# Kernel tuning notes

Hardware: AMD Instinct MI355X
Metric: run time of the kernel (lower is better)

Reference implementation:

```python
import jax, jax.numpy as jnp
import numpy as np

N = 100000
E = 1600000
IN_C = 128
HID = 32
HEADS = 4
OUT_C = 16
G = 128
NEG_SLOPE = 0.2


def setup_inputs() -> dict:
    key = jax.random.key(0)
    ks = jax.random.split(key, 16)
    x = jax.random.normal(ks[0], (N, IN_C), dtype=jnp.float32)
    edge_index = jax.random.randint(ks[1], (2, E), 0, N, dtype=jnp.int64)
    batch = jnp.sort(jax.random.randint(ks[2], (N,), 0, G, dtype=jnp.int64))
    node_weights = jax.random.uniform(ks[3], (N, 1), dtype=jnp.float32)
    s = 1.0 / np.sqrt(IN_C)
    W1 = jax.random.uniform(ks[4], (IN_C, HEADS * HID), jnp.float32, -s, s)
    att_src1 = jax.random.uniform(ks[5], (HEADS, HID), jnp.float32, -s, s)
    att_dst1 = jax.random.uniform(ks[6], (HEADS, HID), jnp.float32, -s, s)
    b1 = jnp.zeros((HEADS * HID,), jnp.float32)
    s2 = 1.0 / np.sqrt(HEADS * HID)
    W2 = jax.random.uniform(ks[7], (HEADS * HID, HID), jnp.float32, -s2, s2)
    att_src2 = jax.random.uniform(ks[8], (1, HID), jnp.float32, -s2, s2)
    att_dst2 = jax.random.uniform(ks[9], (1, HID), jnp.float32, -s2, s2)
    b2 = jnp.zeros((HID,), jnp.float32)
    s3 = 1.0 / np.sqrt(HID)
    fcW = jax.random.uniform(ks[10], (HID, OUT_C), jnp.float32, -s3, s3)
    fcb = jax.random.uniform(ks[11], (OUT_C,), jnp.float32, -s3, s3)
    return {"x": x, "edge_index": edge_index, "batch": batch,
            "node_weights": node_weights,
            "W1": W1, "att_src1": att_src1, "att_dst1": att_dst1, "b1": b1,
            "W2": W2, "att_src2": att_src2, "att_dst2": att_dst2, "b2": b2,
            "fcW": fcW, "fcb": fcb}


def gat_conv(x, src, dst, W, att_src, att_dst, bias, heads, ch, concat):
    n = x.shape[0]
    h = (x @ W).reshape(n, heads, ch)                       # [N,H,C]
    a_src = jnp.sum(h * att_src[None], axis=-1)             # [N,H]
    a_dst = jnp.sum(h * att_dst[None], axis=-1)             # [N,H]
    e = jax.nn.leaky_relu(a_src[src] + a_dst[dst], NEG_SLOPE)  # [E,H]
    # segment softmax over incoming edges of each destination node
    e_max = jax.ops.segment_max(e, dst, num_segments=n)
    ex = jnp.exp(e - e_max[dst])
    denom = jax.ops.segment_sum(ex, dst, num_segments=n)
    alpha = ex / denom[dst]                                 # [E,H]
    msg = h[src] * alpha[..., None]                         # [E,H,C]
    out = jax.ops.segment_sum(msg, dst, num_segments=n)     # [N,H,C]
    if concat:
        out = out.reshape(n, heads * ch)
    else:
        out = out.mean(axis=1)
    return out + bias


def reference(x, edge_index, batch, node_weights,
              W1, att_src1, att_dst1, b1,
              W2, att_src2, att_dst2, b2,
              fcW, fcb):
    n = x.shape[0]
    # PyG GATConv adds self-loops by default
    loop = jnp.arange(n, dtype=edge_index.dtype)
    src = jnp.concatenate([edge_index[0], loop])
    dst = jnp.concatenate([edge_index[1], loop])

    h = x * node_weights
    h = jax.nn.elu(gat_conv(h, src, dst, W1, att_src1, att_dst1, b1, HEADS, HID, True))
    h = jax.nn.elu(gat_conv(h, src, dst, W2, att_src2, att_dst2, b2, 1, HID, False))
    # global mean pool over graphs
    sums = jax.ops.segment_sum(h, batch, num_segments=G)
    cnts = jax.ops.segment_sum(jnp.ones((n,), h.dtype), batch, num_segments=G)
    pooled = sums / jnp.maximum(cnts, 1.0)[:, None]
    return pooled @ fcW + fcb
```

## Files before the change

### kernel.cpp

```cpp
#include <hip/hip_runtime.h>
#include <cstdint>

#define NGRAPH 128
#define NEG 0.2f
#define NB_MAX 512
#define BSH 8
#define BSZ 256
#define CAP 8192
#define BINCH 2048

typedef unsigned int uint;
typedef unsigned short ushort;
typedef unsigned char uchar;
typedef __attribute__((ext_vector_type(8))) short bf16x8;
typedef __attribute__((ext_vector_type(4))) float f32x4;
typedef __attribute__((ext_vector_type(2))) float f32x2;

union U4B { uint4 u; bf16x8 v; };

__device__ __forceinline__ ushort f2bf(float f) {
  uint u = __float_as_uint(f);
  uint r = (u + 0x7FFF + ((u >> 16) & 1)) >> 16;
  return (ushort)r;
}

__device__ __forceinline__ int wave_incl_scan_i(int v) {
  int lane = threadIdx.x & 63;
#pragma unroll
  for (int off = 1; off < 64; off <<= 1) {
    int u = __shfl_up(v, off, 64);
    if (lane >= off) v += u;
  }
  return v;
}

__global__ void k_bin(const int* __restrict__ ei,
                      const float* __restrict__ W1, const float* __restrict__ W2,
                      ushort* __restrict__ Wt1, ushort* __restrict__ Wt2,
                      int E, int Etot, int NB, int nbin,
                      int* __restrict__ bcur, uint* __restrict__ bbuf) {
  if (blockIdx.x >= (uint)nbin) {
    int t2 = (blockIdx.x - nbin) * 256 + threadIdx.x;
    if (t2 < 16384) {
      int n = t2 >> 7, k = t2 & 127;
      Wt1[t2] = f2bf(W1[k * 128 + n]);
    } else {
      int u = t2 - 16384;
      int n = u >> 7, k = u & 127;
      Wt2[u] = f2bf(W2[k * 32 + n]);
    }
    return;
  }
  __shared__ int h[NB_MAX];
  __shared__ int baseo[NB_MAX];
  int t = threadIdx.x;
  for (int b = t; b < NB; b += 256) h[b] = 0;
  int cbase = blockIdx.x * BINCH;
  int myd[8], mys[8];
#pragma unroll
  for (int j = 0; j < 8; j++) {
    int e = cbase + j * 256 + t;
    if (e < Etot) {
      if (e < E) { mys[j] = ei[e]; myd[j] = ei[E + e]; }
      else { mys[j] = e - E; myd[j] = e - E; }
    } else { myd[j] = -1; mys[j] = 0; }
  }
  __syncthreads();
#pragma unroll
  for (int j = 0; j < 8; j++)
    if (myd[j] >= 0) atomicAdd(&h[myd[j] >> BSH], 1);
  __syncthreads();
  for (int b = t; b < NB; b += 256) {
    int c = h[b];
    baseo[b] = c ? atomicAdd(&bcur[b], c) : 0;
    h[b] = 0;
  }
  __syncthreads();
#pragma unroll
  for (int j = 0; j < 8; j++) {
    if (myd[j] >= 0) {
      int b = myd[j] >> BSH;
      int r = atomicAdd(&h[b], 1);
      bbuf[(size_t)b * CAP + baseo[b] + r] =
          ((uint)(myd[j] & (BSZ - 1)) << 17) | (uint)mys[j];
    }
  }
}

__global__ void k_bg(const uint* __restrict__ bbuf, const int* __restrict__ bcur,
                     int NB, int N, int* __restrict__ offs, int* __restrict__ ssrc,
                     const float* __restrict__ x, const ushort* __restrict__ Wt,
                     const float* __restrict__ nw, const float* __restrict__ att_s,
                     const float* __restrict__ att_d, uchar* __restrict__ hb1,
                     float* __restrict__ asrc, float* __restrict__ adst) {
  __shared__ int sst[NB_MAX + 1];
  __shared__ int wsum2[4];
  __shared__ int deg[BSZ];
  if (blockIdx.x < (uint)NB) {
    int t = threadIdx.x, lane = t & 63, wid = t >> 6;
    int v0 = (2 * t < NB) ? bcur[2 * t] : 0;
    int v1 = (2 * t + 1 < NB) ? bcur[2 * t + 1] : 0;
    int s = v0 + v1;
    int sv = wave_incl_scan_i(s);
    if (lane == 63) wsum2[wid] = sv;
    deg[t] = 0;
    __syncthreads();
    if (t == 0) {
      int r = 0;
#pragma unroll
      for (int k = 0; k < 4; k++) { int x2 = wsum2[k]; wsum2[k] = r; r += x2; }
    }
    __syncthreads();
    int excl = wsum2[wid] + sv - s;
    sst[2 * t] = excl;
    sst[2 * t + 1] = excl + v0;
    if (t == 255) sst[512] = excl + v0 + v1;
    __syncthreads();
    int b = blockIdx.x;
    int ebeg = sst[b], eend = sst[b + 1];
    int cnt = eend - ebeg;
    for (int i = t; i < cnt; i += BSZ)
      atomicAdd(&deg[bbuf[(size_t)b * CAP + i] >> 17], 1);
    __syncthreads();
    int v = deg[t];
    int sv2 = wave_incl_scan_i(v);
    if (lane == 63) wsum2[wid] = sv2;
    __syncthreads();
    if (t == 0) {
      int r = 0;
#pragma unroll
      for (int k = 0; k < 4; k++) { int x2 = wsum2[k]; wsum2[k] = r; r += x2; }
    }
    __syncthreads();
    int excl2 = wsum2[wid] + sv2 - v;
    int node = (b << BSH) + t;
    if (node < N) offs[node] = ebeg + excl2;
    if (b == 0 && t == 0) offs[N] = sst[512];
    __syncthreads();
    deg[t] = excl2;
    __syncthreads();
    for (int i = t; i < cnt; i += BSZ) {
      uint rec = bbuf[(size_t)b * CAP + i];
      int r = atomicAdd(&deg[rec >> 17], 1);
      ssrc[ebeg + r] = (int)(rec & 0x1FFFF);
    }
    return;
  }
  int bid = blockIdx.x - NB;
  int wv = threadIdx.x >> 6, l = threadIdx.x & 63;
  int lg = l >> 4, lr = l & 15;
  int row0 = bid * 64 + wv * 16;
  int node = row0 + lr;
  bool valid = node < N;
  float sc = valid ? nw[node] : 0.f;
  bf16x8 xfr[4];
  const float* xr = x + (size_t)node * 128;
#pragma unroll
  for (int kc = 0; kc < 4; kc++) {
    float v[8];
    if (valid) {
      float4 q0 = *reinterpret_cast<const float4*>(xr + kc * 32 + lg * 8);
      float4 q1 = *reinterpret_cast<const float4*>(xr + kc * 32 + lg * 8 + 4);
      v[0] = q0.x; v[1] = q0.y; v[2] = q0.z; v[3] = q0.w;
      v[4] = q1.x; v[5] = q1.y; v[6] = q1.z; v[7] = q1.w;
    } else {
#pragma unroll
      for (int j = 0; j < 8; j++) v[j] = 0.f;
    }
    U4B a;
    uint pk0 = (uint)f2bf(v[0] * sc) | ((uint)f2bf(v[1] * sc) << 16);
    uint pk1 = (uint)f2bf(v[2] * sc) | ((uint)f2bf(v[3] * sc) << 16);
    uint pk2 = (uint)f2bf(v[4] * sc) | ((uint)f2bf(v[5] * sc) << 16);
    uint pk3 = (uint)f2bf(v[6] * sc) | ((uint)f2bf(v[7] * sc) << 16);
    a.u = make_uint4(pk0, pk1, pk2, pk3);
    xfr[kc] = a.v;
  }
  float pS[4] = {}, pD[4] = {};
#pragma unroll
  for (int ct = 0; ct < 8; ct++) {
    f32x4 acc = {0.f, 0.f, 0.f, 0.f};
    const ushort* wrow = Wt + (size_t)(ct * 16 + lr) * 128;
#pragma unroll
    for (int kc = 0; kc < 4; kc++) {
      U4B bfr;
      bfr.u = *reinterpret_cast<const uint4*>(wrow + kc * 32 + lg * 8);
      acc = __builtin_amdgcn_mfma_f32_16x16x32_bf16(bfr.v, xfr[kc], acc, 0, 0, 0);
    }
    int c0 = ct * 16 + lg * 4;
    if (valid) {
      uint u8 = (uint)__builtin_amdgcn_cvt_pk_fp8_f32(acc[0], acc[1], 0, false);
      u8 = (uint)__builtin_amdgcn_cvt_pk_fp8_f32(acc[2], acc[3], u8, true);
      *reinterpret_cast<uint*>(hb1 + (size_t)node * 128 + c0) = u8;
    }
    float4 as4 = *reinterpret_cast<const float4*>(att_s + c0);
    float4 ad4 = *reinterpret_cast<const float4*>(att_d + c0);
    int h = ct >> 1;
    pS[h] += acc[0] * as4.x + acc[1] * as4.y + acc[2] * as4.z + acc[3] * as4.w;
    pD[h] += acc[0] * ad4.x + acc[1] * ad4.y + acc[2] * ad4.z + acc[3] * ad4.w;
  }
#pragma unroll
  for (int off = 16; off < 64; off <<= 1) {
#pragma unroll
    for (int h = 0; h < 4; h++) {
      pS[h] += __shfl_xor(pS[h], off, 64);
      pD[h] += __shfl_xor(pD[h], off, 64);
    }
  }
  if (lg == 0 && valid) {
    *reinterpret_cast<float4*>(asrc + node * 4) = make_float4(pS[0], pS[1], pS[2], pS[3]);
    *reinterpret_cast<float4*>(adst + node * 4) = make_float4(pD[0], pD[1], pD[2], pD[3]);
  }
}

__global__ void k_aggr1(const int* __restrict__ offs, const int* __restrict__ ssrc,
                        const uchar* __restrict__ hb, const float* __restrict__ asrc,
                        const float* __restrict__ adst, const float* __restrict__ bias,
                        const ushort* __restrict__ Wt2, const float* __restrict__ as2,
                        const float* __restrict__ ad2, uchar* __restrict__ hb2,
                        float* __restrict__ asrc2, float* __restrict__ adst2, int N) {
  __shared__ ushort rowl[4][160];
  int tid = threadIdx.x;
  int wv = tid >> 6, l = tid & 63;
  int d = blockIdx.x * 4 + wv;
  int dc = min(d, N - 1);
  int slot = l >> 3;
  int cb = l & 7;
  int h = cb >> 1;
  float ad = adst[dc * 4 + h];
  int beg = offs[dc], end = offs[dc + 1];
  float a[16] = {};
  float ds = 0.f;
  for (int i = beg; i < end; i += 8) {
    int e = i + slot;
    int ec = min(e, end - 1);
    int s = ssrc[ec];
    float xv = asrc[s * 4 + h] + ad;
    xv = xv > 0.f ? xv : NEG * xv;
    float w = __expf(xv);
    w = (e < end) ? w : 0.f;
    uint4 p = *reinterpret_cast<const uint4*>(hb + (size_t)s * 128 + cb * 16);
    uint pu[4] = {p.x, p.y, p.z, p.w};
#pragma unroll
    for (int q = 0; q < 4; q++) {
      f32x2 f0 = __builtin_amdgcn_cvt_pk_f32_fp8(pu[q], false);
      f32x2 f1 = __builtin_amdgcn_cvt_pk_f32_fp8(pu[q], true);
      a[q * 4 + 0] += w * f0.x;
      a[q * 4 + 1] += w * f0.y;
      a[q * 4 + 2] += w * f1.x;
      a[q * 4 + 3] += w * f1.y;
    }
    ds += w;
  }
  int b3 = (l >> 3) & 1, b4 = (l >> 4) & 1, b5 = (l >> 5) & 1;
  float t8[8];
#pragma unroll
  for (int r = 0; r < 8; r++) {
    float send = b3 ? a[r] : a[r + 8];
    float recv = __shfl_xor(send, 8, 64);
    t8[r] = (b3 ? a[r + 8] : a[r]) + recv;
  }
  float t4[4];
#pragma unroll
  for (int r = 0; r < 4; r++) {
    float send = b4 ? t8[r] : t8[r + 4];
    float recv = __shfl_xor(send, 16, 64);
    t4[r] = (b4 ? t8[r + 4] : t8[r]) + recv;
  }
  float t2[2];
#pragma unroll
  for (int r = 0; r < 2; r++) {
    float send = b5 ? t4[r] : t4[r + 2];
    float recv = __shfl_xor(send, 32, 64);
    t2[r] = (b5 ? t4[r + 2] : t4[r]) + recv;
  }
  ds += __shfl_xor(ds, 8, 64);
  ds += __shfl_xor(ds, 16, 64);
  ds += __shfl_xor(ds, 32, 64);
  float inv = 1.f / (ds > 0.f ? ds : 1.f);
  int c0 = cb * 16 + b3 * 8 + b4 * 4 + b5 * 2;
  float r0 = t2[0] * inv + bias[c0];
  float r1 = t2[1] * inv + bias[c0 + 1];
  r0 = r0 > 0.f ? r0 : expm1f(r0);
  r1 = r1 > 0.f ? r1 : expm1f(r1);
  *reinterpret_cast<uint*>(&rowl[wv][c0]) = (uint)f2bf(r0) | ((uint)f2bf(r1) << 16);
  __syncthreads();
  if (wv != 0) return;
  int lg = l >> 4, lr = l & 15;
  int rsel = lr & 3;
  bf16x8 bfrag[4];
#pragma unroll
  for (int kc = 0; kc < 4; kc++) {
    U4B bb;
    bb.u = *reinterpret_cast<const uint4*>(&rowl[rsel][kc * 32 + lg * 8]);
    bfrag[kc] = bb.v;
  }
  int dd = blockIdx.x * 4 + lr;
  bool vs = (lr < 4) && (dd < N);
  float pS = 0.f, pD = 0.f;
#pragma unroll
  for (int ct = 0; ct < 2; ct++) {
    f32x4 acc = {0.f, 0.f, 0.f, 0.f};
    const ushort* wrow = Wt2 + (size_t)(ct * 16 + lr) * 128;
#pragma unroll
    for (int kc = 0; kc < 4; kc++) {
      U4B bfr;
      bfr.u = *reinterpret_cast<const uint4*>(wrow + kc * 32 + lg * 8);
      acc = __builtin_amdgcn_mfma_f32_16x16x32_bf16(bfr.v, bfrag[kc], acc, 0, 0, 0);
    }
    int cg = ct * 16 + lg * 4;
    if (vs) {
      uint u8 = (uint)__builtin_amdgcn_cvt_pk_fp8_f32(acc[0], acc[1], 0, false);
      u8 = (uint)__builtin_amdgcn_cvt_pk_fp8_f32(acc[2], acc[3], u8, true);
      *reinterpret_cast<uint*>(hb2 + (size_t)dd * 32 + cg) = u8;
    }
    float4 as4 = *reinterpret_cast<const float4*>(as2 + cg);
    float4 ad4 = *reinterpret_cast<const float4*>(ad2 + cg);
    pS += acc[0] * as4.x + acc[1] * as4.y + acc[2] * as4.z + acc[3] * as4.w;
    pD += acc[0] * ad4.x + acc[1] * ad4.y + acc[2] * ad4.z + acc[3] * ad4.w;
  }
  pS += __shfl_xor(pS, 16, 64);
  pS += __shfl_xor(pS, 32, 64);
  pD += __shfl_xor(pD, 16, 64);
  pD += __shfl_xor(pD, 32, 64);
  if (vs && lg == 0) { asrc2[dd] = pS; adst2[dd] = pD; }
}

__global__ void k_aggr2(const int* __restrict__ offs, const int* __restrict__ ssrc,
                        const uchar* __restrict__ hb, const float* __restrict__ asrc,
                        const float* __restrict__ adst, const float* __restrict__ bias,
                        float* __restrict__ out, int N) {
  int wid = threadIdx.x >> 6, l = threadIdx.x & 63;
  int d = blockIdx.x * 4 + wid;
  if (d >= N) return;
  int slot = l >> 2;
  int k = l & 3;
  float ad = adst[d];
  int beg = offs[d], end = offs[d + 1];
  float a[8] = {};
  float ds = 0.f;
  for (int i = beg; i < end; i += 16) {
    int e = i + slot;
    int ec = min(e, end - 1);
    int s = ssrc[ec];
    float xv = asrc[s] + ad;
    xv = xv > 0.f ? xv : NEG * xv;
    float w = __expf(xv);
    w = (e < end) ? w : 0.f;
    uint2 p = *reinterpret_cast<const uint2*>(hb + (size_t)s * 32 + k * 8);
    f32x2 f0 = __builtin_amdgcn_cvt_pk_f32_fp8(p.x, false);
    f32x2 f1 = __builtin_amdgcn_cvt_pk_f32_fp8(p.x, true);
    f32x2 f2 = __builtin_amdgcn_cvt_pk_f32_fp8(p.y, false);
    f32x2 f3 = __builtin_amdgcn_cvt_pk_f32_fp8(p.y, true);
    a[0] += w * f0.x; a[1] += w * f0.y; a[2] += w * f1.x; a[3] += w * f1.y;
    a[4] += w * f2.x; a[5] += w * f2.y; a[6] += w * f3.x; a[7] += w * f3.y;
    ds += w;
  }
  int b2 = (l >> 2) & 1, b3 = (l >> 3) & 1, b4 = (l >> 4) & 1;
  float t4[4];
#pragma unroll
  for (int r = 0; r < 4; r++) {
    float send = b2 ? a[r] : a[r + 4];
    float recv = __shfl_xor(send, 4, 64);
    t4[r] = (b2 ? a[r + 4] : a[r]) + recv;
  }
  float t2[2];
#pragma unroll
  for (int r = 0; r < 2; r++) {
    float send = b3 ? t4[r] : t4[r + 2];
    float recv = __shfl_xor(send, 8, 64);
    t2[r] = (b3 ? t4[r + 2] : t4[r]) + recv;
  }
  float send = b4 ? t2[0] : t2[1];
  float recv = __shfl_xor(send, 16, 64);
  float t1 = (b4 ? t2[1] : t2[0]) + recv;
  t1 += __shfl_xor(t1, 32, 64);
  ds += __shfl_xor(ds, 4, 64);
  ds += __shfl_xor(ds, 8, 64);
  ds += __shfl_xor(ds, 16, 64);
  ds += __shfl_xor(ds, 32, 64);
  if (l < 32) {
    int c = k * 8 + b2 * 4 + b3 * 2 + b4;
    float r = t1 / ds + bias[c];
    r = r > 0.f ? r : expm1f(r);
    out[(size_t)d * 32 + c] = r;
  }
}

__global__ void k_pool_fc(const float* __restrict__ h2, const int* __restrict__ batch,
                          const float* __restrict__ fcW, const float* __restrict__ fcb,
                          float* __restrict__ out, int N) {
  int g = blockIdx.x;
  int lo = 0, hi = N;
  while (lo < hi) { int mid = (lo + hi) >> 1; if (batch[mid] < g) lo = mid + 1; else hi = mid; }
  int beg = lo;
  hi = N;
  while (lo < hi) { int mid = (lo + hi) >> 1; if (batch[mid] < g + 1) lo = mid + 1; else hi = mid; }
  int end = lo;
  int t = threadIdx.x, c = t & 31, sub = t >> 5;
  float acc = 0.f;
  for (int n = beg + sub; n < end; n += 8) acc += h2[(size_t)n * 32 + c];
  __shared__ float red[8][32];
  __shared__ float pooled[32];
  red[sub][c] = acc;
  __syncthreads();
  if (sub == 0) {
    float s = 0.f;
#pragma unroll
    for (int i = 0; i < 8; i++) s += red[i][c];
    float cnt = (float)(end - beg);
    pooled[c] = s / fmaxf(cnt, 1.f);
  }
  __syncthreads();
  if (t < 16) {
    float r = fcb[t];
#pragma unroll
    for (int cc = 0; cc < 32; cc++) r += pooled[cc] * fcW[cc * 16 + t];
    out[g * 16 + t] = r;
  }
}

extern "C" void kernel_launch(void* const* d_in, const int* in_sizes, int n_in,
                              void* d_out, int out_size, void* d_ws, size_t ws_size,
                              hipStream_t stream) {
  const float* x     = (const float*)d_in[0];
  const int*   ei    = (const int*)d_in[1];
  const int*   batch = (const int*)d_in[2];
  const float* nw    = (const float*)d_in[3];
  const float* W1    = (const float*)d_in[4];
  const float* as1w  = (const float*)d_in[5];
  const float* ad1w  = (const float*)d_in[6];
  const float* b1    = (const float*)d_in[7];
  const float* W2    = (const float*)d_in[8];
  const float* as2w  = (const float*)d_in[9];
  const float* ad2w  = (const float*)d_in[10];
  const float* b2    = (const float*)d_in[11];
  const float* fcW   = (const float*)d_in[12];
  const float* fcb   = (const float*)d_in[13];
  float* out = (float*)d_out;

  const int N = in_sizes[0] / 128;
  const int E = in_sizes[1] / 2;
  const int Etot = E + N;
  const int NB = (N + BSZ - 1) >> BSH;

  char* w = (char*)d_ws;
  size_t ofs = 0;
  auto alloc = [&](size_t bytes) {
    char* p = w + ofs;
    ofs += (bytes + 255) & ~(size_t)255;
    return p;
  };
  uchar*  hb1    = (uchar*)alloc((size_t)N * 128);
  uchar*  hb2    = (uchar*)alloc((size_t)N * 32);
  float*  h2     = (float*)alloc((size_t)N * 32 * 4);
  float*  asrc1  = (float*)alloc((size_t)N * 4 * 4);
  float*  adst1  = (float*)alloc((size_t)N * 4 * 4);
  float*  asrc2  = (float*)alloc((size_t)N * 4);
  float*  adst2  = (float*)alloc((size_t)N * 4);
  ushort* Wt1    = (ushort*)alloc(16384 * 2);
  ushort* Wt2    = (ushort*)alloc(4096 * 2);
  int*    bcur   = (int*)alloc((size_t)NB * 4);
  int*    offs   = (int*)alloc((size_t)(N + 1) * 4);
  uint*   bbuf   = (uint*)alloc((size_t)NB * CAP * 4);
  int*    ssrc   = (int*)alloc((size_t)Etot * 4);

  hipMemsetAsync(bcur, 0, (size_t)NB * 4, stream);

  const int nbin = (Etot + BINCH - 1) / BINCH;
  k_bin<<<nbin + 80, 256, 0, stream>>>(ei, W1, W2, Wt1, Wt2, E, Etot, NB, nbin, bcur, bbuf);

  const int ngemm1 = (N + 63) / 64;
  k_bg<<<NB + ngemm1, 256, 0, stream>>>(bbuf, bcur, NB, N, offs, ssrc,
                                        x, Wt1, nw, as1w, ad1w, hb1, asrc1, adst1);

  k_aggr1<<<(N + 3) / 4, 256, 0, stream>>>(offs, ssrc, hb1, asrc1, adst1, b1,
                                           Wt2, as2w, ad2w, hb2, asrc2, adst2, N);

  k_aggr2<<<(N + 3) / 4, 256, 0, stream>>>(offs, ssrc, hb2, asrc2, adst2, b2, h2, N);

  k_pool_fc<<<NGRAPH, 256, 0, stream>>>(h2, batch, fcW, fcb, out, N);
}
```

Before: 314.1 us.

## Fuse global mean pool and FC into aggr2 via atomics and last-block reduction

Instead of writing the full layer-2 activations to memory and running a separate pooling kernel, each node's result is atomically added into a per-graph pooled buffer. A global counter identifies the last block, which computes graph counts and applies the final linear layer. This removes the 12.8 MB intermediate write/read and one launch. In exchange it adds heavy atomic contention, because the sorted batch makes nearby nodes hit the same graph addresses, and it makes the summation order nondeterministic.

```diff
diff --git a/kernel.cpp b/kernel.cpp
--- a/kernel.cpp
+++ b/kernel.cpp
@@ -2,6 +2,7 @@
 #include <cstdint>
 
 #define NGRAPH 128
+#define OUT_C 16
 #define NEG 0.2f
 #define NB_MAX 512
 #define BSH 8
@@ -328,94 +329,100 @@
 __global__ void k_aggr2(const int* __restrict__ offs, const int* __restrict__ ssrc,
                         const uchar* __restrict__ hb, const float* __restrict__ asrc,
                         const float* __restrict__ adst, const float* __restrict__ bias,
-                        float* __restrict__ out, int N) {
+                        const int* __restrict__ batch, const float* __restrict__ fcW,
+                        const float* __restrict__ fcb, float* __restrict__ pooled,
+                        int* __restrict__ counter, float* __restrict__ out,
+                        int N, int nblk) {
+  __shared__ float pl[NGRAPH * 32];
+  __shared__ float cnts[NGRAPH];
+  __shared__ int lastf;
   int wid = threadIdx.x >> 6, l = threadIdx.x & 63;
   int d = blockIdx.x * 4 + wid;
-  if (d >= N) return;
-  int slot = l >> 2;
-  int k = l & 3;
-  float ad = adst[d];
-  int beg = offs[d], end = offs[d + 1];
-  float a[8] = {};
-  float ds = 0.f;
-  for (int i = beg; i < end; i += 16) {
-    int e = i + slot;
-    int ec = min(e, end - 1);
-    int s = ssrc[ec];
-    float xv = asrc[s] + ad;
-    xv = xv > 0.f ? xv : NEG * xv;
-    float w = __expf(xv);
-    w = (e < end) ? w : 0.f;
-    uint2 p = *reinterpret_cast<const uint2*>(hb + (size_t)s * 32 + k * 8);
-    f32x2 f0 = __builtin_amdgcn_cvt_pk_f32_fp8(p.x, false);
-    f32x2 f1 = __builtin_amdgcn_cvt_pk_f32_fp8(p.x, true);
-    f32x2 f2 = __builtin_amdgcn_cvt_pk_f32_fp8(p.y, false);
-    f32x2 f3 = __builtin_amdgcn_cvt_pk_f32_fp8(p.y, true);
-    a[0] += w * f0.x; a[1] += w * f0.y; a[2] += w * f1.x; a[3] += w * f1.y;
-    a[4] += w * f2.x; a[5] += w * f2.y; a[6] += w * f3.x; a[7] += w * f3.y;
-    ds += w;
-  }
-  int b2 = (l >> 2) & 1, b3 = (l >> 3) & 1, b4 = (l >> 4) & 1;
-  float t4[4];
-#pragma unroll
-  for (int r = 0; r < 4; r++) {
-    float send = b2 ? a[r] : a[r + 4];
-    float recv = __shfl_xor(send, 4, 64);
-    t4[r] = (b2 ? a[r + 4] : a[r]) + recv;
-  }
-  float t2[2];
-#pragma unroll
-  for (int r = 0; r < 2; r++) {
-    float send = b3 ? t4[r] : t4[r + 2];
-    float recv = __shfl_xor(send, 8, 64);
-    t2[r] = (b3 ? t4[r + 2] : t4[r]) + recv;
-  }
-  float send = b4 ? t2[0] : t2[1];
-  float recv = __shfl_xor(send, 16, 64);
-  float t1 = (b4 ? t2[1] : t2[0]) + recv;
-  t1 += __shfl_xor(t1, 32, 64);
-  ds += __shfl_xor(ds, 4, 64);
-  ds += __shfl_xor(ds, 8, 64);
-  ds += __shfl_xor(ds, 16, 64);
-  ds += __shfl_xor(ds, 32, 64);
-  if (l < 32) {
-    int c = k * 8 + b2 * 4 + b3 * 2 + b4;
-    float r = t1 / ds + bias[c];
-    r = r > 0.f ? r : expm1f(r);
-    out[(size_t)d * 32 + c] = r;
-  }
-}
-
-__global__ void k_pool_fc(const float* __restrict__ h2, const int* __restrict__ batch,
-                          const float* __restrict__ fcW, const float* __restrict__ fcb,
-                          float* __restrict__ out, int N) {
-  int g = blockIdx.x;
-  int lo = 0, hi = N;
-  while (lo < hi) { int mid = (lo + hi) >> 1; if (batch[mid] < g) lo = mid + 1; else hi = mid; }
-  int beg = lo;
-  hi = N;
-  while (lo < hi) { int mid = (lo + hi) >> 1; if (batch[mid] < g + 1) lo = mid + 1; else hi = mid; }
-  int end = lo;
-  int t = threadIdx.x, c = t & 31, sub = t >> 5;
-  float acc = 0.f;
-  for (int n = beg + sub; n < end; n += 8) acc += h2[(size_t)n * 32 + c];
-  __shared__ float red[8][32];
-  __shared__ float pooled[32];
-  red[sub][c] = acc;
-  __syncthreads();
-  if (sub == 0) {
-    float s = 0.f;
-#pragma unroll
-    for (int i = 0; i < 8; i++) s += red[i][c];
-    float cnt = (float)(end - beg);
-    pooled[c] = s / fmaxf(cnt, 1.f);
-  }
-  __syncthreads();
-  if (t < 16) {
-    float r = fcb[t];
-#pragma unroll
-    for (int cc = 0; cc < 32; cc++) r += pooled[cc] * fcW[cc * 16 + t];
-    out[g * 16 + t] = r;
+  if (d < N) {
+    int slot = l >> 2;
+    int k = l & 3;
+    float ad = adst[d];
+    int beg = offs[d], end = offs[d + 1];
+    float a[8] = {};
+    float ds = 0.f;
+    for (int i = beg; i < end; i += 16) {
+      int e = i + slot;
+      int ec = min(e, end - 1);
+      int s = ssrc[ec];
+      float xv = asrc[s] + ad;
+      xv = xv > 0.f ? xv : NEG * xv;
+      float w = __expf(xv);
+      w = (e < end) ? w : 0.f;
+      uint2 p = *reinterpret_cast<const uint2*>(hb + (size_t)s * 32 + k * 8);
+      f32x2 f0 = __builtin_amdgcn_cvt_pk_f32_fp8(p.x, false);
+      f32x2 f1 = __builtin_amdgcn_cvt_pk_f32_fp8(p.x, true);
+      f32x2 f2 = __builtin_amdgcn_cvt_pk_f32_fp8(p.y, false);
+      f32x2 f3 = __builtin_amdgcn_cvt_pk_f32_fp8(p.y, true);
+      a[0] += w * f0.x; a[1] += w * f0.y; a[2] += w * f1.x; a[3] += w * f1.y;
+      a[4] += w * f2.x; a[5] += w * f2.y; a[6] += w * f3.x; a[7] += w * f3.y;
+      ds += w;
+    }
+    int b2 = (l >> 2) & 1, b3 = (l >> 3) & 1, b4 = (l >> 4) & 1;
+    float t4[4];
+#pragma unroll
+    for (int r = 0; r < 4; r++) {
+      float send = b2 ? a[r] : a[r + 4];
+      float recv = __shfl_xor(send, 4, 64);
+      t4[r] = (b2 ? a[r + 4] : a[r]) + recv;
+    }
+    float t2[2];
+#pragma unroll
+    for (int r = 0; r < 2; r++) {
+      float send = b3 ? t4[r] : t4[r + 2];
+      float recv = __shfl_xor(send, 8, 64);
+      t2[r] = (b3 ? t4[r + 2] : t4[r]) + recv;
+    }
+    float send = b4 ? t2[0] : t2[1];
+    float recv = __shfl_xor(send, 16, 64);
+    float t1 = (b4 ? t2[1] : t2[0]) + recv;
+    t1 += __shfl_xor(t1, 32, 64);
+    ds += __shfl_xor(ds, 4, 64);
+    ds += __shfl_xor(ds, 8, 64);
+    ds += __shfl_xor(ds, 16, 64);
+    ds += __shfl_xor(ds, 32, 64);
+    if (l < 32) {
+      int c = k * 8 + b2 * 4 + b3 * 2 + b4;
+      float r = t1 / ds + bias[c];
+      r = r > 0.f ? r : expm1f(r);
+      int g = batch[d];
+      atomicAdd(&pooled[g * 32 + c], r);
+    }
+  }
+  __syncthreads();
+  if (threadIdx.x == 0) {
+    __threadfence();
+    int v = atomicAdd(counter, 1);
+    lastf = (v == nblk - 1);
+  }
+  __syncthreads();
+  if (!lastf) return;
+  __threadfence();
+  int t = threadIdx.x;
+  for (int i = t; i < NGRAPH * 32; i += 256)
+    pl[i] = atomicAdd(&pooled[i], 0.f);
+  if (t < NGRAPH) {
+    int g = t;
+    int lo = 0, hi = N;
+    while (lo < hi) { int mid = (lo + hi) >> 1; if (batch[mid] < g) lo = mid + 1; else hi = mid; }
+    int bg = lo;
+    hi = N;
+    while (lo < hi) { int mid = (lo + hi) >> 1; if (batch[mid] < g + 1) lo = mid + 1; else hi = mid; }
+    cnts[g] = fmaxf((float)(lo - bg), 1.f);
+  }
+  __syncthreads();
+  for (int pair = t; pair < NGRAPH * OUT_C; pair += 256) {
+    int g = pair >> 4, oc = pair & 15;
+    float ic = 1.f / cnts[g];
+    float acc = fcb[oc];
+#pragma unroll
+    for (int cc = 0; cc < 32; cc++)
+      acc += pl[g * 32 + cc] * ic * fcW[cc * 16 + oc];
+    out[g * 16 + oc] = acc;
   }
 }
 
@@ -452,19 +459,21 @@
   };
   uchar*  hb1    = (uchar*)alloc((size_t)N * 128);
   uchar*  hb2    = (uchar*)alloc((size_t)N * 32);
-  float*  h2     = (float*)alloc((size_t)N * 32 * 4);
   float*  asrc1  = (float*)alloc((size_t)N * 4 * 4);
   float*  adst1  = (float*)alloc((size_t)N * 4 * 4);
   float*  asrc2  = (float*)alloc((size_t)N * 4);
   float*  adst2  = (float*)alloc((size_t)N * 4);
   ushort* Wt1    = (ushort*)alloc(16384 * 2);
   ushort* Wt2    = (ushort*)alloc(4096 * 2);
-  int*    bcur   = (int*)alloc((size_t)NB * 4);
+  int*    zbase  = (int*)alloc((size_t)(NB + 8 + NGRAPH * 32) * 4);
+  int*    bcur   = zbase;
+  int*    counter= zbase + NB;
+  float*  pooled = (float*)(zbase + NB + 8);
   int*    offs   = (int*)alloc((size_t)(N + 1) * 4);
   uint*   bbuf   = (uint*)alloc((size_t)NB * CAP * 4);
   int*    ssrc   = (int*)alloc((size_t)Etot * 4);
 
-  hipMemsetAsync(bcur, 0, (size_t)NB * 4, stream);
+  hipMemsetAsync(zbase, 0, (size_t)(NB + 8 + NGRAPH * 32) * 4, stream);
 
   const int nbin = (Etot + BINCH - 1) / BINCH;
   k_bin<<<nbin + 80, 256, 0, stream>>>(ei, W1, W2, Wt1, Wt2, E, Etot, NB, nbin, bcur, bbuf);
@@ -476,7 +485,7 @@
   k_aggr1<<<(N + 3) / 4, 256, 0, stream>>>(offs, ssrc, hb1, asrc1, adst1, b1,
                                            Wt2, as2w, ad2w, hb2, asrc2, adst2, N);
 
-  k_aggr2<<<(N + 3) / 4, 256, 0, stream>>>(offs, ssrc, hb2, asrc2, adst2, b2, h2, N);
-
-  k_pool_fc<<<NGRAPH, 256, 0, stream>>>(h2, batch, fcW, fcb, out, N);
-}
+  const int nblk2 = (N + 3) / 4;
+  k_aggr2<<<nblk2, 256, 0, stream>>>(offs, ssrc, hb2, asrc2, adst2, b2,
+                                     batch, fcW, fcb, pooled, counter, out, N, nblk2);
+}
```

Measured after the change: 864.6 us. 2.75x slower.
